# Performance work log

Hardware: AMD Instinct MI355X
Metric: run time of the kernel (lower is better)

## Reference

```python
import jax, jax.numpy as jnp
import numpy as np

IH, IW = 48, 48           # img_size
C = 256                   # inp == oup
NH, HD = 8, 32            # num_heads, head_dims; inner_dim = 256
HID = 4 * C               # MLP hidden
N = IH * IW               # window size (seq len) = 2304
SCALE = (C // NH) ** -0.5 # (inp_dims // num_heads) ** -0.5
EPS = 1e-5


def _relative_position_index():
    coords = np.stack(np.meshgrid(np.arange(IH), np.arange(IW), indexing='ij'))
    cf = coords.reshape(2, -1)
    rel = (cf[:, :, None] - cf[:, None, :]).transpose(1, 2, 0)
    rel[:, :, 0] += IH - 1
    rel[:, :, 1] += IW - 1
    rel[:, :, 0] *= 2 * IW - 1
    return jnp.asarray(rel.sum(-1).astype(np.int32))  # [N, N]


def setup_inputs() -> dict:
    key = jax.random.key(0)
    ks = jax.random.split(key, 12)
    s = 0.02
    return {
        'x': jax.random.normal(ks[0], (1, IH, IW, C), jnp.float32),
        'gamma1': jnp.ones((C,), jnp.float32),
        'beta1': jnp.zeros((C,), jnp.float32),
        'w_qkv': jax.random.normal(ks[1], (C, 3 * NH * HD), jnp.float32) * s,
        'w_proj': jax.random.normal(ks[2], (NH * HD, C), jnp.float32) * s,
        'b_proj': jnp.zeros((C,), jnp.float32),
        'bias_table': jax.random.normal(ks[3], ((2 * IH - 1) * (2 * IW - 1), NH), jnp.float32) * s,
        'gamma2': jnp.ones((C,), jnp.float32),
        'beta2': jnp.zeros((C,), jnp.float32),
        'w_fc1': jax.random.normal(ks[4], (C, HID), jnp.float32) * s,
        'b_fc1': jnp.zeros((HID,), jnp.float32),
        'w_fc2': jax.random.normal(ks[5], (HID, C), jnp.float32) * s,
        'b_fc2': jnp.zeros((C,), jnp.float32),
        'rel_idx': _relative_position_index(),
    }


def _layernorm(x, g, b):
    mu = jnp.mean(x, axis=-1, keepdims=True)
    var = jnp.mean(jnp.square(x - mu), axis=-1, keepdims=True)
    return (x - mu) * jax.lax.rsqrt(var + EPS) * g + b


def reference(x, gamma1, beta1, w_qkv, w_proj, b_proj, bias_table,
              gamma2, beta2, w_fc1, b_fc1, w_fc2, b_fc2, rel_idx):
    shortcut = x                                   # [1, IH, IW, C]
    t = x.reshape(1, N, C)
    t = _layernorm(t, gamma1, beta1)

    # qkv: [1, N, 3*NH*HD] -> q, k, v each [1, NH, N, HD]
    qkv = (t @ w_qkv).reshape(1, N, 3, NH, HD).transpose(2, 0, 3, 1, 4)
    q, k, v = qkv[0], qkv[1], qkv[2]
    q = q * SCALE

    attn = jnp.einsum('bhnd,bhmd->bhnm', q, k)     # [1, NH, N, N]
    # relative position bias: gather table rows by index -> [NH, N, N]
    bias = bias_table[rel_idx.reshape(-1)].reshape(N, N, NH).transpose(2, 0, 1)
    attn = jax.nn.softmax(attn + bias[None], axis=-1)

    o = jnp.einsum('bhnm,bhmd->bhnd', attn, v)     # [1, NH, N, HD]
    o = o.transpose(0, 2, 1, 3).reshape(1, N, NH * HD)
    o = o @ w_proj + b_proj                        # [1, N, C]

    x = shortcut + o.reshape(1, IH, IW, C)
    shortcut = x

    t = _layernorm(x.reshape(1, N, C), gamma2, beta2)
    t = jax.nn.gelu(t @ w_fc1 + b_fc1, approximate=False) @ w_fc2 + b_fc2
    return shortcut + t.reshape(1, IH, IW, C)
```

## Files before the change

### kernel.cpp

```cpp
#include <hip/hip_runtime.h>
#include <hip/hip_bf16.h>
#include <math.h>

#define IH 48
#define IW 48
#define NN 2304
#define CC 256
#define NH 8
#define HD 32
#define HID 1024
#define NBIAS 9025
#define SCALE 0.17677669529663687f
#define LN_EPS 1e-5f

typedef __attribute__((ext_vector_type(8))) short bf16x8;
typedef __attribute__((ext_vector_type(4))) float f32x4;

__device__ __forceinline__ short f2b(float f) {
    __hip_bfloat16 h = __float2bfloat16(f);
    short s; __builtin_memcpy(&s, &h, 2); return s;
}
__device__ __forceinline__ float b2f(short s) {
    __hip_bfloat16 h; __builtin_memcpy(&h, &s, 2); return __bfloat162float(h);
}

__global__ void prep_kernel(const float* __restrict__ x, const float* __restrict__ g,
                            const float* __restrict__ b, short* __restrict__ t1,
                            const float* __restrict__ w_qkv, const float* __restrict__ w_proj,
                            const float* __restrict__ w_fc1, const float* __restrict__ w_fc2,
                            const float* __restrict__ bt,
                            short* __restrict__ o_qkv, short* __restrict__ o_proj,
                            short* __restrict__ o_fc1, short* __restrict__ o_fc2,
                            short* __restrict__ o_bias)
{
    const int bid = blockIdx.x, tid = threadIdx.x;
    if (bid < NN) {
        __shared__ float red[8];
        float v = x[bid * CC + tid];
        float s = v, s2 = v * v;
        #pragma unroll
        for (int off = 32; off > 0; off >>= 1) {
            s  += __shfl_xor(s, off);
            s2 += __shfl_xor(s2, off);
        }
        const int wid = tid >> 6;
        if ((tid & 63) == 0) { red[wid * 2] = s; red[wid * 2 + 1] = s2; }
        __syncthreads();
        float tot  = red[0] + red[2] + red[4] + red[6];
        float tot2 = red[1] + red[3] + red[5] + red[7];
        float mu   = tot * (1.0f / CC);
        float var  = tot2 * (1.0f / CC) - mu * mu;
        float rstd = rsqrtf(var + LN_EPS);
        t1[bid * CC + tid] = f2b((v - mu) * rstd * g[tid] + b[tid]);
        return;
    }
    const int stride = (gridDim.x - NN) * 256;
    for (int i = (bid - NN) * 256 + tid; i < 858632; i += stride) {
        int j = i;
        if (j < 196608)            { int n = j >> 8,  k = j & 255;  o_qkv [j] = f2b(w_qkv [k * 768  + n]); }
        else if ((j -= 196608) < 65536)  { int n = j >> 8,  k = j & 255;  o_proj[j] = f2b(w_proj[k * 256  + n]); }
        else if ((j -= 65536)  < 262144) { int n = j >> 8,  k = j & 255;  o_fc1 [j] = f2b(w_fc1 [k * 1024 + n]); }
        else if ((j -= 262144) < 262144) { int n = j >> 10, k = j & 1023; o_fc2 [j] = f2b(w_fc2 [k * 256  + n]); }
        else { j -= 262144; int h = j / NBIAS, idx = j - h * NBIAS; o_bias[j] = f2b(bt[idx * NH + h]); }
    }
}

__global__ void ln_kernel(const float* __restrict__ x,
                          const float* __restrict__ g,
                          const float* __restrict__ b,
                          short* __restrict__ out)
{
    __shared__ float red[8];
    const int row = blockIdx.x, tid = threadIdx.x;
    float v = x[row * CC + tid];
    float s = v, s2 = v * v;
    #pragma unroll
    for (int off = 32; off > 0; off >>= 1) {
        s  += __shfl_xor(s, off);
        s2 += __shfl_xor(s2, off);
    }
    const int wid = tid >> 6;
    if ((tid & 63) == 0) { red[wid * 2] = s; red[wid * 2 + 1] = s2; }
    __syncthreads();
    float tot  = red[0] + red[2] + red[4] + red[6];
    float tot2 = red[1] + red[3] + red[5] + red[7];
    float mu   = tot * (1.0f / CC);
    float var  = tot2 * (1.0f / CC) - mu * mu;
    float rstd = rsqrtf(var + LN_EPS);
    out[row * CC + tid] = f2b((v - mu) * rstd * g[tid] + b[tid]);
}

#define GSTRIDE 72
template<int K>
__device__ __forceinline__ void mfma_gemm_core(const short* __restrict__ A,
                                               const short* __restrict__ BT,
                                               int m0, int n0, f32x4 acc[4],
                                               short* lds)
{
    short* As = lds;
    short* Bs = lds + 64 * GSTRIDE;
    const int tid  = threadIdx.x;
    const int w    = tid >> 6, lane = tid & 63;
    const int quad = lane >> 4, l15 = lane & 15;
    const int sr = tid >> 2;
    const int sc = (tid & 3) * 16;
    #pragma unroll
    for (int c = 0; c < 4; ++c) acc[c] = (f32x4){0.f, 0.f, 0.f, 0.f};

    const short* Ap = &A [(m0 + sr) * K + sc];
    const short* Bp = &BT[(n0 + sr) * K + sc];
    bf16x8 ra0 = *(const bf16x8*)Ap,       ra1 = *(const bf16x8*)(Ap + 8);
    bf16x8 rb0 = *(const bf16x8*)Bp,       rb1 = *(const bf16x8*)(Bp + 8);

    for (int k0 = 0; k0 < K; k0 += 64) {
        __syncthreads();
        *(bf16x8*)&As[sr * GSTRIDE + sc]     = ra0;
        *(bf16x8*)&As[sr * GSTRIDE + sc + 8] = ra1;
        *(bf16x8*)&Bs[sr * GSTRIDE + sc]     = rb0;
        *(bf16x8*)&Bs[sr * GSTRIDE + sc + 8] = rb1;
        if (k0 + 64 < K) {
            ra0 = *(const bf16x8*)(Ap + k0 + 64);
            ra1 = *(const bf16x8*)(Ap + k0 + 72);
            rb0 = *(const bf16x8*)(Bp + k0 + 64);
            rb1 = *(const bf16x8*)(Bp + k0 + 72);
        }
        __syncthreads();
        #pragma unroll
        for (int s = 0; s < 2; ++s) {
            bf16x8 a = *(const bf16x8*)&As[(w * 16 + l15) * GSTRIDE + s * 32 + quad * 8];
            #pragma unroll
            for (int c = 0; c < 4; ++c) {
                bf16x8 b = *(const bf16x8*)&Bs[(c * 16 + l15) * GSTRIDE + s * 32 + quad * 8];
                acc[c] = __builtin_amdgcn_mfma_f32_16x16x32_bf16(a, b, acc[c], 0, 0, 0);
            }
        }
    }
}

__global__ void qkv_kernel(const short* __restrict__ t1, const short* __restrict__ wT,
                           short* __restrict__ qb, short* __restrict__ kb,
                           short* __restrict__ vT)
{
    __shared__ short lds[2 * 64 * GSTRIDE];
    f32x4 acc[4];
    const int m0 = blockIdx.y * 64, n0 = blockIdx.x * 64;
    mfma_gemm_core<256>(t1, wT, m0, n0, acc, lds);
    const int lane = threadIdx.x & 63, w = threadIdx.x >> 6;
    const int quad = lane >> 4, l15 = lane & 15;
    #pragma unroll
    for (int c = 0; c < 4; ++c) {
        int col = n0 + c * 16 + l15;
        int three = col >> 8, rem = col & 255;
        int h = rem >> 5, d = rem & 31;
        #pragma unroll
        for (int r = 0; r < 4; ++r) {
            int row = m0 + w * 16 + quad * 4 + r;
            float v = acc[c][r];
            if (three == 0)      qb[(h * NN + row) * HD + d] = f2b(v * SCALE);
            else if (three == 1) kb[(h * NN + row) * HD + d] = f2b(v);
            else                 vT[(h * HD + d) * NN + row] = f2b(v);
        }
    }
}

#define PSTRIDE 40
__global__ __launch_bounds__(512) void attn_kernel(
        const short* __restrict__ qb, const short* __restrict__ kb,
        const short* __restrict__ vT, const short* __restrict__ biasT,
        short* __restrict__ o)
{
    __shared__ float Ored[8][16][33];
    __shared__ float lred[8][16];
    __shared__ short sbuf[8][16 * PSTRIDE];
    const int w = threadIdx.x >> 6, lane = threadIdx.x & 63;
    const int quad = lane >> 4, l15 = lane & 15;
    const int h = blockIdx.x / 144, q0 = (blockIdx.x % 144) * 16;
    const int t0 = w * 288;
    short* sb = &sbuf[w][0];
    const short* bt = &biasT[h * NBIAS];

    bf16x8 qf = *(const bf16x8*)&qb[(h * NN + q0 + l15) * HD + quad * 8];

    int base[4];
    #pragma unroll
    for (int r = 0; r < 4; ++r) {
        int row = q0 + quad * 4 + r;
        int qi = row / IW, qj = row % IW;
        base[r] = (qi + 47) * 95 + (qj + 47);
    }

    f32x4 O0 = (f32x4){0.f,0.f,0.f,0.f}, O1 = (f32x4){0.f,0.f,0.f,0.f};
    float lp[4] = {0.f, 0.f, 0.f, 0.f};
    const f32x4 zero = (f32x4){0.f,0.f,0.f,0.f};

    for (int c = 0; c < 9; ++c) {
        const int t = t0 + c * 32;
        bf16x8 k0f = *(const bf16x8*)&kb[(h * NN + t      + l15) * HD + quad * 8];
        bf16x8 k1f = *(const bf16x8*)&kb[(h * NN + t + 16 + l15) * HD + quad * 8];
        f32x4 s0 = __builtin_amdgcn_mfma_f32_16x16x32_bf16(qf, k0f, zero, 0, 0, 0);
        f32x4 s1 = __builtin_amdgcn_mfma_f32_16x16x32_bf16(qf, k1f, zero, 0, 0, 0);
        bf16x8 v0 = *(const bf16x8*)&vT[(h * HD + l15)      * NN + t + quad * 8];
        bf16x8 v1 = *(const bf16x8*)&vT[(h * HD + 16 + l15) * NN + t + quad * 8];

        int key0 = t + l15, key1 = t + 16 + l15;
        int boff0 = -((key0 / IW) * 95 + key0 % IW);
        int boff1 = -((key1 / IW) * 95 + key1 % IW);

        #pragma unroll
        for (int r = 0; r < 4; ++r) {
            float p0 = __expf(s0[r] + b2f(bt[base[r] + boff0]));
            float p1 = __expf(s1[r] + b2f(bt[base[r] + boff1]));
            lp[r] += p0 + p1;
            sb[(quad * 4 + r) * PSTRIDE + l15]      = f2b(p0);
            sb[(quad * 4 + r) * PSTRIDE + 16 + l15] = f2b(p1);
        }
        asm volatile("s_waitcnt lgkmcnt(0)" ::: "memory");
        bf16x8 pa = *(const bf16x8*)&sb[l15 * PSTRIDE + quad * 8];
        O0 = __builtin_amdgcn_mfma_f32_16x16x32_bf16(pa, v0, O0, 0, 0, 0);
        O1 = __builtin_amdgcn_mfma_f32_16x16x32_bf16(pa, v1, O1, 0, 0, 0);
    }

    #pragma unroll
    for (int r = 0; r < 4; ++r) {
        float l = lp[r];
        l += __shfl_xor(l, 1); l += __shfl_xor(l, 2);
        l += __shfl_xor(l, 4); l += __shfl_xor(l, 8);
        if (l15 == 0) lred[w][quad * 4 + r] = l;
        Ored[w][quad * 4 + r][l15]      = O0[r];
        Ored[w][quad * 4 + r][16 + l15] = O1[r];
    }
    __syncthreads();
    {
        int rr  = 2 * w + (lane >> 5);
        int col = lane & 31;
        float s = 0.f, l = 0.f;
        #pragma unroll
        for (int p = 0; p < 8; ++p) { s += Ored[p][rr][col]; l += lred[p][rr]; }
        o[(q0 + rr) * CC + h * HD + col] = f2b(s / l);
    }
}

__global__ void proj_kernel(const short* __restrict__ o, const short* __restrict__ wT,
                            const float* __restrict__ bias, const float* __restrict__ x_in,
                            float* __restrict__ x2)
{
    __shared__ short lds[2 * 64 * GSTRIDE];
    f32x4 acc[4];
    const int m0 = blockIdx.y * 64, n0 = blockIdx.x * 64;
    mfma_gemm_core<256>(o, wT, m0, n0, acc, lds);
    const int lane = threadIdx.x & 63, w = threadIdx.x >> 6;
    const int quad = lane >> 4, l15 = lane & 15;
    #pragma unroll
    for (int c = 0; c < 4; ++c) {
        int col = n0 + c * 16 + l15;
        #pragma unroll
        for (int r = 0; r < 4; ++r) {
            int row = m0 + w * 16 + quad * 4 + r;
            x2[row * CC + col] = acc[c][r] + bias[col] + x_in[row * CC + col];
        }
    }
}

__global__ void fc1_kernel(const short* __restrict__ t2, const short* __restrict__ wT,
                           const float* __restrict__ bias, short* __restrict__ h1)
{
    __shared__ short lds[2 * 64 * GSTRIDE];
    f32x4 acc[4];
    const int m0 = blockIdx.y * 64, n0 = blockIdx.x * 64;
    mfma_gemm_core<256>(t2, wT, m0, n0, acc, lds);
    const int lane = threadIdx.x & 63, w = threadIdx.x >> 6;
    const int quad = lane >> 4, l15 = lane & 15;
    #pragma unroll
    for (int c = 0; c < 4; ++c) {
        int col = n0 + c * 16 + l15;
        #pragma unroll
        for (int r = 0; r < 4; ++r) {
            int row = m0 + w * 16 + quad * 4 + r;
            float v = acc[c][r] + bias[col];
            float ge = 0.5f * v * (1.0f + erff(v * 0.7071067811865476f));
            h1[row * HID + col] = f2b(ge);
        }
    }
}

__global__ void fc2_kernel(const short* __restrict__ h1, const short* __restrict__ wT,
                           const float* __restrict__ bias, const float* __restrict__ x2,
                           float* __restrict__ out)
{
    __shared__ short lds[2 * 64 * GSTRIDE];
    f32x4 acc[4];
    const int m0 = blockIdx.y * 64, n0 = blockIdx.x * 64;
    mfma_gemm_core<1024>(h1, wT, m0, n0, acc, lds);
    const int lane = threadIdx.x & 63, w = threadIdx.x >> 6;
    const int quad = lane >> 4, l15 = lane & 15;
    #pragma unroll
    for (int c = 0; c < 4; ++c) {
        int col = n0 + c * 16 + l15;
        #pragma unroll
        for (int r = 0; r < 4; ++r) {
            int row = m0 + w * 16 + quad * 4 + r;
            out[row * CC + col] = acc[c][r] + bias[col] + x2[row * CC + col];
        }
    }
}

extern "C" void kernel_launch(void* const* d_in, const int* in_sizes, int n_in,
                              void* d_out, int out_size, void* d_ws, size_t ws_size,
                              hipStream_t stream)
{
    const float* x          = (const float*)d_in[0];
    const float* gamma1     = (const float*)d_in[1];
    const float* beta1      = (const float*)d_in[2];
    const float* w_qkv      = (const float*)d_in[3];
    const float* w_proj     = (const float*)d_in[4];
    const float* b_proj     = (const float*)d_in[5];
    const float* bias_table = (const float*)d_in[6];
    const float* gamma2     = (const float*)d_in[7];
    const float* beta2      = (const float*)d_in[8];
    const float* w_fc1      = (const float*)d_in[9];
    const float* b_fc1      = (const float*)d_in[10];
    const float* w_fc2      = (const float*)d_in[11];
    const float* b_fc2      = (const float*)d_in[12];

    short* S = (short*)d_ws;
    const int NC = NN * CC;
    short* t1     = S;
    short* qb     = t1  + NC;
    short* kb     = qb  + NC;
    short* vT     = kb  + NC;
    short* obuf   = vT  + NC;
    short* t2     = obuf+ NC;
    short* h1     = t2  + NC;
    short* wTqkv  = h1  + NN * HID;
    short* wTproj = wTqkv  + 768 * 256;
    short* wTfc1  = wTproj + 256 * 256;
    short* wTfc2  = wTfc1  + 1024 * 256;
    short* biasT  = wTfc2  + 256 * 1024;
    float* x2     = (float*)(biasT + NH * NBIAS + 8);

    prep_kernel<<<NN + 512, 256, 0, stream>>>(x, gamma1, beta1, t1,
                                              w_qkv, w_proj, w_fc1, w_fc2, bias_table,
                                              wTqkv, wTproj, wTfc1, wTfc2, biasT);
    qkv_kernel<<<dim3(12, 36), 256, 0, stream>>>(t1, wTqkv, qb, kb, vT);
    attn_kernel<<<1152, 512, 0, stream>>>(qb, kb, vT, biasT, obuf);
    proj_kernel<<<dim3(4, 36), 256, 0, stream>>>(obuf, wTproj, b_proj, x, x2);
    ln_kernel<<<NN, 256, 0, stream>>>(x2, gamma2, beta2, t2);
    fc1_kernel<<<dim3(16, 36), 256, 0, stream>>>(t2, wTfc1, b_fc1, h1);
    fc2_kernel<<<dim3(4, 36), 256, 0, stream>>>(h1, wTfc2, b_fc2, x2,
                                                (float*)d_out);
}
```

Before: 164.7 us.

## Split-K proj/fc2 with atomics, exp2 softmax, halve attention block waves

Proj and fc2 GEMMs now use split-K over a z grid dimension, accumulating with float atomicAdd into outputs that are pre-seeded with the residual plus bias by the prep and LN kernels. Softmax switches to exp2, with log2e folded into the Q scale and the bias table. The attention kernel drops from 8 to 4 waves per block, each covering twice as many key chunks, which halves its shared-memory reduction buffers. Together these aim to raise GEMM parallelism for the narrow-N layers and cut exp cost, at the price of atomic traffic, non-deterministic summation order, and fewer waves per attention block.

```diff
diff --git a/kernel.cpp b/kernel.cpp
--- a/kernel.cpp
+++ b/kernel.cpp
@@ -11,6 +11,7 @@
 #define HID 1024
 #define NBIAS 9025
 #define SCALE 0.17677669529663687f
+#define LOG2E 1.4426950408889634f
 #define LN_EPS 1e-5f
 
 typedef __attribute__((ext_vector_type(8))) short bf16x8;
@@ -23,9 +24,17 @@
 __device__ __forceinline__ float b2f(short s) {
     __hip_bfloat16 h; __builtin_memcpy(&h, &s, 2); return __bfloat162float(h);
 }
+__device__ __forceinline__ float fast_exp2(float x) {
+#if __has_builtin(__builtin_amdgcn_exp2f)
+    return __builtin_amdgcn_exp2f(x);
+#else
+    return exp2f(x);
+#endif
+}
 
 __global__ void prep_kernel(const float* __restrict__ x, const float* __restrict__ g,
-                            const float* __restrict__ b, short* __restrict__ t1,
+                            const float* __restrict__ b, const float* __restrict__ bp,
+                            short* __restrict__ t1, float* __restrict__ x2,
                             const float* __restrict__ w_qkv, const float* __restrict__ w_proj,
                             const float* __restrict__ w_fc1, const float* __restrict__ w_fc2,
                             const float* __restrict__ bt,
@@ -52,6 +61,7 @@
         float var  = tot2 * (1.0f / CC) - mu * mu;
         float rstd = rsqrtf(var + LN_EPS);
         t1[bid * CC + tid] = f2b((v - mu) * rstd * g[tid] + b[tid]);
+        x2[bid * CC + tid] = v + bp[tid];
         return;
     }
     const int stride = (gridDim.x - NN) * 256;
@@ -61,14 +71,16 @@
         else if ((j -= 196608) < 65536)  { int n = j >> 8,  k = j & 255;  o_proj[j] = f2b(w_proj[k * 256  + n]); }
         else if ((j -= 65536)  < 262144) { int n = j >> 8,  k = j & 255;  o_fc1 [j] = f2b(w_fc1 [k * 1024 + n]); }
         else if ((j -= 262144) < 262144) { int n = j >> 10, k = j & 1023; o_fc2 [j] = f2b(w_fc2 [k * 256  + n]); }
-        else { j -= 262144; int h = j / NBIAS, idx = j - h * NBIAS; o_bias[j] = f2b(bt[idx * NH + h]); }
+        else { j -= 262144; int h = j / NBIAS, idx = j - h * NBIAS; o_bias[j] = f2b(bt[idx * NH + h] * LOG2E); }
     }
 }
 
 __global__ void ln_kernel(const float* __restrict__ x,
                           const float* __restrict__ g,
                           const float* __restrict__ b,
-                          short* __restrict__ out)
+                          const float* __restrict__ bfc2,
+                          short* __restrict__ out_t,
+                          float* __restrict__ out_base)
 {
     __shared__ float red[8];
     const int row = blockIdx.x, tid = threadIdx.x;
@@ -87,14 +99,15 @@
     float mu   = tot * (1.0f / CC);
     float var  = tot2 * (1.0f / CC) - mu * mu;
     float rstd = rsqrtf(var + LN_EPS);
-    out[row * CC + tid] = f2b((v - mu) * rstd * g[tid] + b[tid]);
+    out_t[row * CC + tid] = f2b((v - mu) * rstd * g[tid] + b[tid]);
+    out_base[row * CC + tid] = v + bfc2[tid];
 }
 
 #define GSTRIDE 72
-template<int K>
+template<int KLEN, int KSTR>
 __device__ __forceinline__ void mfma_gemm_core(const short* __restrict__ A,
                                                const short* __restrict__ BT,
-                                               int m0, int n0, f32x4 acc[4],
+                                               int m0, int n0, int kb, f32x4 acc[4],
                                                short* lds)
 {
     short* As = lds;
@@ -107,18 +120,18 @@
     #pragma unroll
     for (int c = 0; c < 4; ++c) acc[c] = (f32x4){0.f, 0.f, 0.f, 0.f};
 
-    const short* Ap = &A [(m0 + sr) * K + sc];
-    const short* Bp = &BT[(n0 + sr) * K + sc];
+    const short* Ap = &A [(m0 + sr) * KSTR + kb + sc];
+    const short* Bp = &BT[(n0 + sr) * KSTR + kb + sc];
     bf16x8 ra0 = *(const bf16x8*)Ap,       ra1 = *(const bf16x8*)(Ap + 8);
     bf16x8 rb0 = *(const bf16x8*)Bp,       rb1 = *(const bf16x8*)(Bp + 8);
 
-    for (int k0 = 0; k0 < K; k0 += 64) {
+    for (int k0 = 0; k0 < KLEN; k0 += 64) {
         __syncthreads();
         *(bf16x8*)&As[sr * GSTRIDE + sc]     = ra0;
         *(bf16x8*)&As[sr * GSTRIDE + sc + 8] = ra1;
         *(bf16x8*)&Bs[sr * GSTRIDE + sc]     = rb0;
         *(bf16x8*)&Bs[sr * GSTRIDE + sc + 8] = rb1;
-        if (k0 + 64 < K) {
+        if (k0 + 64 < KLEN) {
             ra0 = *(const bf16x8*)(Ap + k0 + 64);
             ra1 = *(const bf16x8*)(Ap + k0 + 72);
             rb0 = *(const bf16x8*)(Bp + k0 + 64);
@@ -144,7 +157,7 @@
     __shared__ short lds[2 * 64 * GSTRIDE];
     f32x4 acc[4];
     const int m0 = blockIdx.y * 64, n0 = blockIdx.x * 64;
-    mfma_gemm_core<256>(t1, wT, m0, n0, acc, lds);
+    mfma_gemm_core<256, 256>(t1, wT, m0, n0, 0, acc, lds);
     const int lane = threadIdx.x & 63, w = threadIdx.x >> 6;
     const int quad = lane >> 4, l15 = lane & 15;
     #pragma unroll
@@ -156,7 +169,7 @@
         for (int r = 0; r < 4; ++r) {
             int row = m0 + w * 16 + quad * 4 + r;
             float v = acc[c][r];
-            if (three == 0)      qb[(h * NN + row) * HD + d] = f2b(v * SCALE);
+            if (three == 0)      qb[(h * NN + row) * HD + d] = f2b(v * (SCALE * LOG2E));
             else if (three == 1) kb[(h * NN + row) * HD + d] = f2b(v);
             else                 vT[(h * HD + d) * NN + row] = f2b(v);
         }
@@ -164,18 +177,18 @@
 }
 
 #define PSTRIDE 40
-__global__ __launch_bounds__(512) void attn_kernel(
+__global__ __launch_bounds__(256) void attn_kernel(
         const short* __restrict__ qb, const short* __restrict__ kb,
         const short* __restrict__ vT, const short* __restrict__ biasT,
         short* __restrict__ o)
 {
-    __shared__ float Ored[8][16][33];
-    __shared__ float lred[8][16];
-    __shared__ short sbuf[8][16 * PSTRIDE];
+    __shared__ float Ored[4][16][33];
+    __shared__ float lred[4][16];
+    __shared__ short sbuf[4][16 * PSTRIDE];
     const int w = threadIdx.x >> 6, lane = threadIdx.x & 63;
     const int quad = lane >> 4, l15 = lane & 15;
     const int h = blockIdx.x / 144, q0 = (blockIdx.x % 144) * 16;
-    const int t0 = w * 288;
+    const int t0 = w * 576;
     short* sb = &sbuf[w][0];
     const short* bt = &biasT[h * NBIAS];
 
@@ -193,7 +206,7 @@
     float lp[4] = {0.f, 0.f, 0.f, 0.f};
     const f32x4 zero = (f32x4){0.f,0.f,0.f,0.f};
 
-    for (int c = 0; c < 9; ++c) {
+    for (int c = 0; c < 18; ++c) {
         const int t = t0 + c * 32;
         bf16x8 k0f = *(const bf16x8*)&kb[(h * NN + t      + l15) * HD + quad * 8];
         bf16x8 k1f = *(const bf16x8*)&kb[(h * NN + t + 16 + l15) * HD + quad * 8];
@@ -208,8 +221,8 @@
 
         #pragma unroll
         for (int r = 0; r < 4; ++r) {
-            float p0 = __expf(s0[r] + b2f(bt[base[r] + boff0]));
-            float p1 = __expf(s1[r] + b2f(bt[base[r] + boff1]));
+            float p0 = fast_exp2(s0[r] + b2f(bt[base[r] + boff0]));
+            float p1 = fast_exp2(s1[r] + b2f(bt[base[r] + boff1]));
             lp[r] += p0 + p1;
             sb[(quad * 4 + r) * PSTRIDE + l15]      = f2b(p0);
             sb[(quad * 4 + r) * PSTRIDE + 16 + l15] = f2b(p1);
@@ -231,43 +244,43 @@
     }
     __syncthreads();
     {
-        int rr  = 2 * w + (lane >> 5);
-        int col = lane & 31;
-        float s = 0.f, l = 0.f;
-        #pragma unroll
-        for (int p = 0; p < 8; ++p) { s += Ored[p][rr][col]; l += lred[p][rr]; }
-        o[(q0 + rr) * CC + h * HD + col] = f2b(s / l);
+        const int col = threadIdx.x & 31;
+        for (int rr = threadIdx.x >> 5; rr < 16; rr += 8) {
+            float s = 0.f, l = 0.f;
+            #pragma unroll
+            for (int p = 0; p < 4; ++p) { s += Ored[p][rr][col]; l += lred[p][rr]; }
+            o[(q0 + rr) * CC + h * HD + col] = f2b(s / l);
+        }
     }
 }
 
 __global__ void proj_kernel(const short* __restrict__ o, const short* __restrict__ wT,
-                            const float* __restrict__ bias, const float* __restrict__ x_in,
                             float* __restrict__ x2)
+{
+    __shared__ short lds[2 * 64 * GSTRIDE];
+    f32x4 acc[4];
+    const int m0 = blockIdx.y * 64, n0 = blockIdx.x * 64, kb = blockIdx.z * 128;
+    mfma_gemm_core<128, 256>(o, wT, m0, n0, kb, acc, lds);
+    const int lane = threadIdx.x & 63, w = threadIdx.x >> 6;
+    const int quad = lane >> 4, l15 = lane & 15;
+    #pragma unroll
+    for (int c = 0; c < 4; ++c) {
+        int col = n0 + c * 16 + l15;
+        #pragma unroll
+        for (int r = 0; r < 4; ++r) {
+            int row = m0 + w * 16 + quad * 4 + r;
+            atomicAdd(&x2[row * CC + col], acc[c][r]);
+        }
+    }
+}
+
+__global__ void fc1_kernel(const short* __restrict__ t2, const short* __restrict__ wT,
+                           const float* __restrict__ bias, short* __restrict__ h1)
 {
     __shared__ short lds[2 * 64 * GSTRIDE];
     f32x4 acc[4];
     const int m0 = blockIdx.y * 64, n0 = blockIdx.x * 64;
-    mfma_gemm_core<256>(o, wT, m0, n0, acc, lds);
-    const int lane = threadIdx.x & 63, w = threadIdx.x >> 6;
-    const int quad = lane >> 4, l15 = lane & 15;
-    #pragma unroll
-    for (int c = 0; c < 4; ++c) {
-        int col = n0 + c * 16 + l15;
-        #pragma unroll
-        for (int r = 0; r < 4; ++r) {
-            int row = m0 + w * 16 + quad * 4 + r;
-            x2[row * CC + col] = acc[c][r] + bias[col] + x_in[row * CC + col];
-        }
-    }
-}
-
-__global__ void fc1_kernel(const short* __restrict__ t2, const short* __restrict__ wT,
-                           const float* __restrict__ bias, short* __restrict__ h1)
-{
-    __shared__ short lds[2 * 64 * GSTRIDE];
-    f32x4 acc[4];
-    const int m0 = blockIdx.y * 64, n0 = blockIdx.x * 64;
-    mfma_gemm_core<256>(t2, wT, m0, n0, acc, lds);
+    mfma_gemm_core<256, 256>(t2, wT, m0, n0, 0, acc, lds);
     const int lane = threadIdx.x & 63, w = threadIdx.x >> 6;
     const int quad = lane >> 4, l15 = lane & 15;
     #pragma unroll
@@ -284,13 +297,12 @@
 }
 
 __global__ void fc2_kernel(const short* __restrict__ h1, const short* __restrict__ wT,
-                           const float* __restrict__ bias, const float* __restrict__ x2,
                            float* __restrict__ out)
 {
     __shared__ short lds[2 * 64 * GSTRIDE];
     f32x4 acc[4];
-    const int m0 = blockIdx.y * 64, n0 = blockIdx.x * 64;
-    mfma_gemm_core<1024>(h1, wT, m0, n0, acc, lds);
+    const int m0 = blockIdx.y * 64, n0 = blockIdx.x * 64, kb = blockIdx.z * 512;
+    mfma_gemm_core<512, 1024>(h1, wT, m0, n0, kb, acc, lds);
     const int lane = threadIdx.x & 63, w = threadIdx.x >> 6;
     const int quad = lane >> 4, l15 = lane & 15;
     #pragma unroll
@@ -299,7 +311,7 @@
         #pragma unroll
         for (int r = 0; r < 4; ++r) {
             int row = m0 + w * 16 + quad * 4 + r;
-            out[row * CC + col] = acc[c][r] + bias[col] + x2[row * CC + col];
+            atomicAdd(&out[row * CC + col], acc[c][r]);
         }
     }
 }
@@ -338,14 +350,13 @@
     short* biasT  = wTfc2  + 256 * 1024;
     float* x2     = (float*)(biasT + NH * NBIAS + 8);
 
-    prep_kernel<<<NN + 512, 256, 0, stream>>>(x, gamma1, beta1, t1,
+    prep_kernel<<<NN + 512, 256, 0, stream>>>(x, gamma1, beta1, b_proj, t1, x2,
                                               w_qkv, w_proj, w_fc1, w_fc2, bias_table,
                                               wTqkv, wTproj, wTfc1, wTfc2, biasT);
     qkv_kernel<<<dim3(12, 36), 256, 0, stream>>>(t1, wTqkv, qb, kb, vT);
-    attn_kernel<<<1152, 512, 0, stream>>>(qb, kb, vT, biasT, obuf);
-    proj_kernel<<<dim3(4, 36), 256, 0, stream>>>(obuf, wTproj, b_proj, x, x2);
-    ln_kernel<<<NN, 256, 0, stream>>>(x2, gamma2, beta2, t2);
+    attn_kernel<<<1152, 256, 0, stream>>>(qb, kb, vT, biasT, obuf);
+    proj_kernel<<<dim3(4, 36, 2), 256, 0, stream>>>(obuf, wTproj, x2);
+    ln_kernel<<<NN, 256, 0, stream>>>(x2, gamma2, beta2, b_fc2, t2, (float*)d_out);
     fc1_kernel<<<dim3(16, 36), 256, 0, stream>>>(t2, wTfc1, b_fc1, h1);
-    fc2_kernel<<<dim3(4, 36), 256, 0, stream>>>(h1, wTfc2, b_fc2, x2,
-                                                (float*)d_out);
-}
+    fc2_kernel<<<dim3(4, 36, 2), 256, 0, stream>>>(h1, wTfc2, (float*)d_out);
+}
```

Measured after the change: 170.9 us. 3.7% more time.
